# Kernel tuning notes

Hardware: AMD Instinct MI355X
Metric: run time of the kernel (lower is better)

Reference implementation:

```python
import jax, jax.numpy as jnp
import numpy as np

K = 4

def grid_sample_bilinear_zeros(img, grid):
    # img: [b,c,H,W]; grid: [b,h,w,2] normalized coords (x,y) in [-1,1]
    # PyTorch grid_sample, mode='bilinear', padding_mode='zeros', align_corners=False
    b, c, H, W = img.shape
    h, w = grid.shape[1], grid.shape[2]
    ix = (grid[..., 0] + 1.0) * (W * 0.5) - 0.5
    iy = (grid[..., 1] + 1.0) * (H * 0.5) - 0.5
    x0 = jnp.floor(ix); y0 = jnp.floor(iy)
    wx1 = ix - x0; wx0 = 1.0 - wx1
    wy1 = iy - y0; wy0 = 1.0 - wy1
    x0i = x0.astype(jnp.int32); y0i = y0.astype(jnp.int32)
    x1i = x0i + 1; y1i = y0i + 1
    imgf = img.reshape(b, c, H * W)
    N = h * w

    def gather(xi, yi, wgt):
        valid = (xi >= 0) & (xi < W) & (yi >= 0) & (yi < H)
        xc = jnp.clip(xi, 0, W - 1); yc = jnp.clip(yi, 0, H - 1)
        idx = (yc * W + xc).reshape(b, 1, N)
        g = jnp.take_along_axis(imgf, jnp.broadcast_to(idx, (b, c, N)), axis=2)
        wv = (wgt * valid.astype(img.dtype)).reshape(b, 1, N)
        return g * wv

    out = (gather(x0i, y0i, wx0 * wy0) + gather(x1i, y0i, wx1 * wy0) +
           gather(x0i, y1i, wx0 * wy1) + gather(x1i, y1i, wx1 * wy1))
    return out.reshape(b, c, h, w)


def setup_inputs() -> dict:
    key = jax.random.key(0)
    ks = jax.random.split(key, 8)
    b, c, h, w = 8, 256, 96, 96
    out_ch = 256
    x = jax.random.normal(ks[0], (b, c, h, w), dtype=jnp.float32)
    Wc = jax.random.normal(ks[1], (out_ch, c), dtype=jnp.float32) * 0.02
    bc = jax.random.normal(ks[2], (out_ch,), dtype=jnp.float32) * 0.02
    Woff = jax.random.normal(ks[3], (K, 2, c), dtype=jnp.float32) * 0.02
    boff = jax.random.normal(ks[4], (K, 2), dtype=jnp.float32) * 0.02
    Wwt = jax.random.normal(ks[5], (K, c), dtype=jnp.float32) * 0.02
    bwt = jax.random.normal(ks[6], (K,), dtype=jnp.float32) * 0.02
    return {"x": x, "Wc": Wc, "bc": bc, "Woff": Woff, "boff": boff, "Wwt": Wwt, "bwt": bwt}


def reference(x, Wc, bc, Woff, boff, Wwt, bwt):
    b, c, h, w = x.shape
    # 1x1 conv projection
    proj = jnp.einsum('bchw,oc->bohw', x, Wc) + bc[None, :, None, None]
    # k flow fields, each [b,2,h,w] -> [k,b,h,w,2]
    flows = jnp.einsum('bchw,koc->kbohw', x, Woff) + boff[:, None, :, None, None]
    flows = jnp.transpose(flows, (0, 1, 3, 4, 2))
    # softmax sampling weights [b,k,h,w]
    logits = jnp.einsum('bchw,kc->bkhw', x, Wwt) + bwt[None, :, None, None]
    weights = jax.nn.softmax(logits, axis=1)
    # base pixel grid (x,y)
    gy, gx = jnp.meshgrid(jnp.arange(h, dtype=x.dtype), jnp.arange(w, dtype=x.dtype), indexing='ij')
    base = jnp.stack((gx, gy), axis=-1)  # [h,w,2]
    vgrid = base[None, None] + flows  # [k,b,h,w,2]
    vx = 2.0 * vgrid[..., 0] / max(w - 1, 1) - 1.0
    vy = 2.0 * vgrid[..., 1] / max(h - 1, 1) - 1.0
    vgrid_scaled = jnp.stack((vx, vy), axis=-1)  # [k,b,h,w,2]
    feats = jax.vmap(lambda g: grid_sample_bilinear_zeros(proj, g))(vgrid_scaled)  # [k,b,o,h,w]
    out = jnp.einsum('kbohw,bkhw->bohw', feats, weights)
    return out
```

## Files before the change

kernel.cpp:

```cpp
#include <hip/hip_runtime.h>

#define HW   9216
#define IMG  96
#define NB   8
#define NK   4

typedef __bf16 bf16x8 __attribute__((ext_vector_type(8)));
typedef float  f32x4  __attribute__((ext_vector_type(4)));

__device__ __forceinline__ unsigned short f2bf(float f) {
    unsigned int u = __float_as_uint(f);
    u += 0x7FFFu + ((u >> 16) & 1u);
    return (unsigned short)(u >> 16);
}

extern "C" __global__ __launch_bounds__(256, 4)
void prep_kernel(const float* __restrict__ x,
                 const float* __restrict__ Wc,
                 const float* __restrict__ Woff,
                 const float* __restrict__ boff,
                 const float* __restrict__ Wwt,
                 const float* __restrict__ bwt,
                 unsigned short* __restrict__ xbt,
                 unsigned short* __restrict__ Wcb,
                 float2* __restrict__ coords,
                 float* __restrict__ wts)
{
    __shared__ __align__(16) unsigned short tile[64 * 264];

    const int t   = threadIdx.x;
    const int bxr = blockIdx.x;

    if (bxr >= NB * 144) {
        int u = ((bxr - NB * 144) * 256 + t) * 4;
        float4 v = *(const float4*)(Wc + u);
        union { unsigned short h[4]; int2 p; } pk;
        pk.h[0] = f2bf(v.x); pk.h[1] = f2bf(v.y);
        pk.h[2] = f2bf(v.z); pk.h[3] = f2bf(v.w);
        *(int2*)(Wcb + u) = pk.p;
        return;
    }

    const int b  = bxr / 144;
    const int p0 = (bxr % 144) * 64;
    const int px = t & 63;
    const int g  = __builtin_amdgcn_readfirstlane(t >> 6);

    float acc[12];
    #pragma unroll
    for (int j = 0; j < 12; ++j) acc[j] = 0.f;

    const float* xb = x + ((size_t)(b * 256 + g * 64)) * HW + p0 + px;
    unsigned int* trow = (unsigned int*)tile;

    for (int i0 = 0; i0 < 64; i0 += 8) {
        float v[8];
        #pragma unroll
        for (int q = 0; q < 8; ++q)
            v[q] = xb[(size_t)(i0 + q) * HW];
        #pragma unroll
        for (int q = 0; q < 8; ++q) {
            const int c = g * 64 + i0 + q;
            #pragma unroll
            for (int j = 0; j < 8; ++j) acc[j] += v[q] * Woff[j * 256 + c];
            #pragma unroll
            for (int j = 0; j < 4; ++j) acc[8 + j] += v[q] * Wwt[j * 256 + c];
        }
        #pragma unroll
        for (int q = 0; q < 8; q += 2) {
            unsigned int pk = (unsigned int)f2bf(v[q]) | ((unsigned int)f2bf(v[q + 1]) << 16);
            trow[px * 132 + ((g * 64 + i0 + q) >> 1)] = pk;
        }
    }

    __syncthreads();
    #pragma unroll
    for (int r = 0; r < 8; ++r) {
        int u = t + 256 * r;
        int sub = u & 31, p2 = u >> 5;
        int4 v = *(const int4*)(tile + p2 * 264 + sub * 8);
        *(int4*)(xbt + ((size_t)b * HW + p0 + p2) * 256 + sub * 8) = v;
    }
    __syncthreads();

    float* red = (float*)tile;
    #pragma unroll
    for (int j = 0; j < 12; ++j)
        red[(g * 64 + px) * 12 + j] = acc[j];
    __syncthreads();

    if (t < 64) {
        float s[12];
        #pragma unroll
        for (int j = 0; j < 12; ++j)
            s[j] = red[(0 * 64 + px) * 12 + j] + red[(1 * 64 + px) * 12 + j] +
                   red[(2 * 64 + px) * 12 + j] + red[(3 * 64 + px) * 12 + j];

        const int p = p0 + px;
        const float pyf = (float)(p / IMG);
        const float pxf = (float)(p % IMG);

        #pragma unroll
        for (int k = 0; k < NK; ++k) {
            float fx = s[k * 2 + 0] + boff[k * 2 + 0];
            float fy = s[k * 2 + 1] + boff[k * 2 + 1];
            float vx = 2.0f * (pxf + fx) / 95.0f - 1.0f;
            float vy = 2.0f * (pyf + fy) / 95.0f - 1.0f;
            float ix = (vx + 1.0f) * 48.0f - 0.5f;
            float iy = (vy + 1.0f) * 48.0f - 0.5f;
            coords[((size_t)k * NB + b) * HW + p] = make_float2(ix, iy);
        }
        float l0 = s[8] + bwt[0], l1 = s[9] + bwt[1];
        float l2 = s[10] + bwt[2], l3 = s[11] + bwt[3];
        float m = fmaxf(fmaxf(l0, l1), fmaxf(l2, l3));
        float e0 = __expf(l0 - m), e1 = __expf(l1 - m);
        float e2 = __expf(l2 - m), e3 = __expf(l3 - m);
        float inv = 1.0f / (e0 + e1 + e2 + e3);
        wts[((size_t)0 * NB + b) * HW + p] = e0 * inv;
        wts[((size_t)1 * NB + b) * HW + p] = e1 * inv;
        wts[((size_t)2 * NB + b) * HW + p] = e2 * inv;
        wts[((size_t)3 * NB + b) * HW + p] = e3 * inv;
    }
}

extern "C" __global__ __launch_bounds__(256)
void sample_kernel(const unsigned short* __restrict__ xbt,
                   const float2* __restrict__ coords,
                   float* __restrict__ wts,
                   unsigned short* __restrict__ xs)
{
    const int t  = threadIdx.x;
    const int b  = blockIdx.x / 1152;
    const int p0 = (blockIdx.x % 1152) * 8;
    const int pxl = t >> 5, ch = t & 31;
    const int p  = p0 + pxl;

    int   idx[16];
    float w[16];
    #pragma unroll
    for (int k = 0; k < NK; ++k) {
        float2 cc = coords[((size_t)k * NB + b) * HW + p];
        float wk  = wts[((size_t)k * NB + b) * HW + p];
        float x0f = floorf(cc.x), y0f = floorf(cc.y);
        float wx1 = cc.x - x0f, wx0 = 1.0f - wx1;
        float wy1 = cc.y - y0f, wy0 = 1.0f - wy1;
        int x0 = (int)x0f, y0 = (int)y0f;
        int x1 = x0 + 1,   y1 = y0 + 1;
        float vx0 = (x0 >= 0 && x0 < IMG) ? 1.f : 0.f;
        float vx1 = (x1 >= 0 && x1 < IMG) ? 1.f : 0.f;
        float vy0 = (y0 >= 0 && y0 < IMG) ? 1.f : 0.f;
        float vy1 = (y1 >= 0 && y1 < IMG) ? 1.f : 0.f;
        int cx0 = min(max(x0, 0), IMG - 1), cx1 = min(max(x1, 0), IMG - 1);
        int cy0 = min(max(y0, 0), IMG - 1), cy1 = min(max(y1, 0), IMG - 1);
        idx[k * 4 + 0] = cy0 * IMG + cx0;  w[k * 4 + 0] = wk * wx0 * wy0 * vx0 * vy0;
        idx[k * 4 + 1] = cy0 * IMG + cx1;  w[k * 4 + 1] = wk * wx1 * wy0 * vx1 * vy0;
        idx[k * 4 + 2] = cy1 * IMG + cx0;  w[k * 4 + 2] = wk * wx0 * wy1 * vx0 * vy1;
        idx[k * 4 + 3] = cy1 * IMG + cx1;  w[k * 4 + 3] = wk * wx1 * wy1 * vx1 * vy1;
    }

    const unsigned short* base = xbt + (size_t)b * HW * 256 + ch * 8;
    float acc[8];
    #pragma unroll
    for (int i = 0; i < 8; ++i) acc[i] = 0.f;

    #pragma unroll
    for (int j = 0; j < 16; ++j) {
        int4 v = *(const int4*)(base + (size_t)idx[j] * 256);
        const unsigned int* u = (const unsigned int*)&v;
        float wj = w[j];
        #pragma unroll
        for (int q = 0; q < 4; ++q) {
            float lo = __uint_as_float(u[q] << 16);
            float hi = __uint_as_float(u[q] & 0xFFFF0000u);
            acc[2 * q + 0] += wj * lo;
            acc[2 * q + 1] += wj * hi;
        }
    }

    union { unsigned short h[8]; int4 v; } pk;
    #pragma unroll
    for (int i = 0; i < 8; ++i) pk.h[i] = f2bf(acc[i]);
    *(int4*)(xs + ((size_t)b * HW + p) * 256 + ch * 8) = pk.v;

    if (ch == 0) {
        float wsum = 0.f;
        #pragma unroll
        for (int j = 0; j < 16; ++j) wsum += w[j];
        wts[(size_t)b * HW + p] = wsum;
    }
}

extern "C" __global__ __launch_bounds__(256)
void gemm_kernel(const unsigned short* __restrict__ Wcb,
                 const unsigned short* __restrict__ xs,
                 const float* __restrict__ bc,
                 const float* __restrict__ wts,
                 float* __restrict__ out)
{
    __shared__ __align__(16) unsigned short As[128 * 32];
    __shared__ __align__(16) unsigned short Bs[128 * 32];

    const int t  = threadIdx.x;
    const int bx = blockIdx.x;
    const int b  = bx / 144;
    const int r  = bx % 144;
    const int m0 = (r / 72) * 128;
    const int p0 = (r % 72) * 128;

    const int lane = t & 63, wave = t >> 6;
    const int wm = (wave >> 1) * 64, wn = (wave & 1) * 64;
    const int l15 = lane & 15, quad = lane >> 4;

    f32x4 acc[4][4];
    #pragma unroll
    for (int mt = 0; mt < 4; ++mt)
        #pragma unroll
        for (int nt = 0; nt < 4; ++nt)
            acc[mt][nt] = (f32x4){0.f, 0.f, 0.f, 0.f};

    const unsigned short* aBase = Wcb + (size_t)m0 * 256;
    const unsigned short* bBase = xs + ((size_t)b * HW + p0) * 256;

    for (int k0 = 0; k0 < 256; k0 += 32) {
        #pragma unroll
        for (int i = 0; i < 2; ++i) {
            int u = t + 256 * i;
            int row = u >> 2, sub = u & 3;
            __builtin_amdgcn_global_load_lds(
                (const __attribute__((address_space(1))) void*)(aBase + (size_t)row * 256 + k0 + sub * 8),
                (__attribute__((address_space(3))) void*)(As + u * 8), 16, 0, 0);
            __builtin_amdgcn_global_load_lds(
                (const __attribute__((address_space(1))) void*)(bBase + (size_t)row * 256 + k0 + sub * 8),
                (__attribute__((address_space(3))) void*)(Bs + u * 8), 16, 0, 0);
        }
        __syncthreads();
        bf16x8 af[4], bf[4];
        #pragma unroll
        for (int mt = 0; mt < 4; ++mt)
            af[mt] = *(const bf16x8*)(const void*)(As + (wm + mt * 16 + l15) * 32 + quad * 8);
        #pragma unroll
        for (int nt = 0; nt < 4; ++nt)
            bf[nt] = *(const bf16x8*)(const void*)(Bs + (wn + nt * 16 + l15) * 32 + quad * 8);
        #pragma unroll
        for (int mt = 0; mt < 4; ++mt)
            #pragma unroll
            for (int nt = 0; nt < 4; ++nt)
                acc[mt][nt] = __builtin_amdgcn_mfma_f32_16x16x32_bf16(af[mt], bf[nt], acc[mt][nt], 0, 0, 0);
        __syncthreads();
    }

    float wv[4];
    #pragma unroll
    for (int nt = 0; nt < 4; ++nt)
        wv[nt] = wts[(size_t)b * HW + p0 + wn + nt * 16 + l15];

    #pragma unroll
    for (int mt = 0; mt < 4; ++mt) {
        int ob = m0 + wm + mt * 16 + quad * 4;
        #pragma unroll
        for (int reg = 0; reg < 4; ++reg) {
            int o = ob + reg;
            float bias = bc[o];
            float* dst = out + ((size_t)b * 256 + o) * HW + p0 + wn + l15;
            #pragma unroll
            for (int nt = 0; nt < 4; ++nt)
                dst[nt * 16] = acc[mt][nt][reg] + bias * wv[nt];
        }
    }
}

extern "C" void kernel_launch(void* const* d_in, const int* in_sizes, int n_in,
                              void* d_out, int out_size, void* d_ws, size_t ws_size,
                              hipStream_t stream)
{
    const float* x    = (const float*)d_in[0];
    const float* Wc   = (const float*)d_in[1];
    const float* bc   = (const float*)d_in[2];
    const float* Woff = (const float*)d_in[3];
    const float* boff = (const float*)d_in[4];
    const float* Wwt  = (const float*)d_in[5];
    const float* bwt  = (const float*)d_in[6];
    float* out = (float*)d_out;

    char* ws = (char*)d_ws;
    unsigned short* xbt  = (unsigned short*)(ws);
    unsigned short* xs   = (unsigned short*)(ws + 37748736);
    float2* coords       = (float2*)(ws + 75497472);
    float*  wts          = (float*)(ws + 77856768);
    unsigned short* Wcb  = (unsigned short*)(ws + 79036416);

    prep_kernel<<<dim3(NB * 144 + 64), dim3(256), 0, stream>>>(
        x, Wc, Woff, boff, Wwt, bwt, xbt, Wcb, coords, wts);
    sample_kernel<<<dim3(NB * 1152), dim3(256), 0, stream>>>(xbt, coords, wts, xs);
    gemm_kernel<<<dim3(NB * 144), dim3(256), 0, stream>>>(Wcb, xs, bc, wts, out);
}
```

Measured before the change: 213.2 us.

## Stage x tiles via global_load_lds and write bf16 transpose directly

The prep kernel now loads x in two 32-channel phases per wave using direct global-to-LDS DMA loads with 16-byte vector accesses instead of strided per-thread scalar loads. Each lane reads its pixel column from LDS, accumulates the offset and weight projections, and writes its packed bf16 channel row straight to global memory. This removes the transposed LDS tile, one sync, and the cooperative copy-out loop. Launch bounds rise to 5 blocks per CU. Each lane's direct store covers only 16 bytes per row, and the hard vmcnt wait leaves the load and compute phases without overlap.

```diff
diff --git a/kernel.cpp b/kernel.cpp
--- a/kernel.cpp
+++ b/kernel.cpp
@@ -14,7 +14,7 @@
     return (unsigned short)(u >> 16);
 }
 
-extern "C" __global__ __launch_bounds__(256, 4)
+extern "C" __global__ __launch_bounds__(256, 5)
 void prep_kernel(const float* __restrict__ x,
                  const float* __restrict__ Wc,
                  const float* __restrict__ Woff,
@@ -26,7 +26,7 @@
                  float2* __restrict__ coords,
                  float* __restrict__ wts)
 {
-    __shared__ __align__(16) unsigned short tile[64 * 264];
+    __shared__ __align__(16) unsigned char lds_raw[32768];
 
     const int t   = threadIdx.x;
     const int bxr = blockIdx.x;
@@ -41,62 +41,70 @@
         return;
     }
 
-    const int b  = bxr / 144;
-    const int p0 = (bxr % 144) * 64;
-    const int px = t & 63;
-    const int g  = __builtin_amdgcn_readfirstlane(t >> 6);
+    const int b    = bxr / 144;
+    const int p0   = (bxr % 144) * 64;
+    const int lane = t & 63;
+    const int g    = __builtin_amdgcn_readfirstlane(t >> 6);
+
+    const float* XAf = (const float*)(lds_raw) + g * 2048;
 
     float acc[12];
     #pragma unroll
     for (int j = 0; j < 12; ++j) acc[j] = 0.f;
 
-    const float* xb = x + ((size_t)(b * 256 + g * 64)) * HW + p0 + px;
-    unsigned int* trow = (unsigned int*)tile;
-
-    for (int i0 = 0; i0 < 64; i0 += 8) {
-        float v[8];
-        #pragma unroll
-        for (int q = 0; q < 8; ++q)
-            v[q] = xb[(size_t)(i0 + q) * HW];
-        #pragma unroll
-        for (int q = 0; q < 8; ++q) {
-            const int c = g * 64 + i0 + q;
+    unsigned short* xrow = xbt + ((size_t)b * HW + p0 + lane) * 256 + g * 64;
+
+    #pragma unroll
+    for (int phase = 0; phase < 2; ++phase) {
+        const int cb = g * 64 + phase * 32;
+
+        #pragma unroll
+        for (int i2 = 0; i2 < 8; ++i2) {
+            const float* src = x + ((size_t)(b * 256 + cb + i2 * 4 + (lane >> 4))) * HW
+                                 + p0 + (lane & 15) * 4;
+            __builtin_amdgcn_global_load_lds(
+                (const __attribute__((address_space(1))) void*)src,
+                (__attribute__((address_space(3))) void*)(lds_raw + g * 8192 + i2 * 1024 + lane * 16),
+                16, 0, 0);
+        }
+        asm volatile("s_waitcnt vmcnt(0)" ::: "memory");
+
+        #pragma unroll
+        for (int s8 = 0; s8 < 4; ++s8) {
+            union { unsigned int u[4]; int4 i4; } pk;
             #pragma unroll
-            for (int j = 0; j < 8; ++j) acc[j] += v[q] * Woff[j * 256 + c];
-            #pragma unroll
-            for (int j = 0; j < 4; ++j) acc[8 + j] += v[q] * Wwt[j * 256 + c];
-        }
-        #pragma unroll
-        for (int q = 0; q < 8; q += 2) {
-            unsigned int pk = (unsigned int)f2bf(v[q]) | ((unsigned int)f2bf(v[q + 1]) << 16);
-            trow[px * 132 + ((g * 64 + i0 + q) >> 1)] = pk;
+            for (int pr = 0; pr < 4; ++pr) {
+                const int r = s8 * 8 + pr * 2;
+                float v0 = XAf[(r + 0) * 64 + lane];
+                float v1 = XAf[(r + 1) * 64 + lane];
+                const int c0 = cb + r, c1 = cb + r + 1;
+                #pragma unroll
+                for (int j = 0; j < 8; ++j)
+                    acc[j] += v0 * Woff[j * 256 + c0] + v1 * Woff[j * 256 + c1];
+                #pragma unroll
+                for (int j = 0; j < 4; ++j)
+                    acc[8 + j] += v0 * Wwt[j * 256 + c0] + v1 * Wwt[j * 256 + c1];
+                pk.u[pr] = (unsigned int)f2bf(v0) | ((unsigned int)f2bf(v1) << 16);
+            }
+            *(int4*)(xrow + phase * 32 + s8 * 8) = pk.i4;
         }
     }
 
     __syncthreads();
-    #pragma unroll
-    for (int r = 0; r < 8; ++r) {
-        int u = t + 256 * r;
-        int sub = u & 31, p2 = u >> 5;
-        int4 v = *(const int4*)(tile + p2 * 264 + sub * 8);
-        *(int4*)(xbt + ((size_t)b * HW + p0 + p2) * 256 + sub * 8) = v;
-    }
-    __syncthreads();
-
-    float* red = (float*)tile;
+    float* red = (float*)lds_raw;
     #pragma unroll
     for (int j = 0; j < 12; ++j)
-        red[(g * 64 + px) * 12 + j] = acc[j];
+        red[(g * 64 + lane) * 12 + j] = acc[j];
     __syncthreads();
 
     if (t < 64) {
         float s[12];
         #pragma unroll
         for (int j = 0; j < 12; ++j)
-            s[j] = red[(0 * 64 + px) * 12 + j] + red[(1 * 64 + px) * 12 + j] +
-                   red[(2 * 64 + px) * 12 + j] + red[(3 * 64 + px) * 12 + j];
-
-        const int p = p0 + px;
+            s[j] = red[(0 * 64 + lane) * 12 + j] + red[(1 * 64 + lane) * 12 + j] +
+                   red[(2 * 64 + lane) * 12 + j] + red[(3 * 64 + lane) * 12 + j];
+
+        const int p = p0 + lane;
         const float pyf = (float)(p / IMG);
         const float pxf = (float)(p % IMG);
 
```

Measured after the change: 232.5 us. 1.09x slower.

## Fuse bilinear sampling into GEMM kernel, staging sampled tile in LDS

Applied to the files above, without the earlier changes.

Merges the sampling kernel into the GEMM: each block computes sampling indices and weights for its 128 pixels, gathers and blends all 256 input channels into a swizzled LDS B tile, then runs the MFMA loop reading only A from global memory. This removes the bf16 intermediate write and re-read and one kernel launch. The cost is that the two output-channel halves each redo the full gather for the same pixels, and the large LDS footprint limits occupancy. XOR swizzles are added to A and B LDS layouts to reduce bank conflicts.

```diff
diff --git a/kernel.cpp b/kernel.cpp
--- a/kernel.cpp
+++ b/kernel.cpp
@@ -123,82 +123,20 @@
     }
 }
 
-extern "C" __global__ __launch_bounds__(256)
-void sample_kernel(const unsigned short* __restrict__ xbt,
-                   const float2* __restrict__ coords,
-                   float* __restrict__ wts,
-                   unsigned short* __restrict__ xs)
+extern "C" __global__ __launch_bounds__(256, 2)
+void fused_kernel(const unsigned short* __restrict__ Wcb,
+                  const unsigned short* __restrict__ xbt,
+                  const float2* __restrict__ coords,
+                  const float* __restrict__ wts,
+                  const float* __restrict__ bc,
+                  float* __restrict__ out)
 {
-    const int t  = threadIdx.x;
-    const int b  = blockIdx.x / 1152;
-    const int p0 = (blockIdx.x % 1152) * 8;
-    const int pxl = t >> 5, ch = t & 31;
-    const int p  = p0 + pxl;
-
-    int   idx[16];
-    float w[16];
-    #pragma unroll
-    for (int k = 0; k < NK; ++k) {
-        float2 cc = coords[((size_t)k * NB + b) * HW + p];
-        float wk  = wts[((size_t)k * NB + b) * HW + p];
-        float x0f = floorf(cc.x), y0f = floorf(cc.y);
-        float wx1 = cc.x - x0f, wx0 = 1.0f - wx1;
-        float wy1 = cc.y - y0f, wy0 = 1.0f - wy1;
-        int x0 = (int)x0f, y0 = (int)y0f;
-        int x1 = x0 + 1,   y1 = y0 + 1;
-        float vx0 = (x0 >= 0 && x0 < IMG) ? 1.f : 0.f;
-        float vx1 = (x1 >= 0 && x1 < IMG) ? 1.f : 0.f;
-        float vy0 = (y0 >= 0 && y0 < IMG) ? 1.f : 0.f;
-        float vy1 = (y1 >= 0 && y1 < IMG) ? 1.f : 0.f;
-        int cx0 = min(max(x0, 0), IMG - 1), cx1 = min(max(x1, 0), IMG - 1);
-        int cy0 = min(max(y0, 0), IMG - 1), cy1 = min(max(y1, 0), IMG - 1);
-        idx[k * 4 + 0] = cy0 * IMG + cx0;  w[k * 4 + 0] = wk * wx0 * wy0 * vx0 * vy0;
-        idx[k * 4 + 1] = cy0 * IMG + cx1;  w[k * 4 + 1] = wk * wx1 * wy0 * vx1 * vy0;
-        idx[k * 4 + 2] = cy1 * IMG + cx0;  w[k * 4 + 2] = wk * wx0 * wy1 * vx0 * vy1;
-        idx[k * 4 + 3] = cy1 * IMG + cx1;  w[k * 4 + 3] = wk * wx1 * wy1 * vx1 * vy1;
-    }
-
-    const unsigned short* base = xbt + (size_t)b * HW * 256 + ch * 8;
-    float acc[8];
-    #pragma unroll
-    for (int i = 0; i < 8; ++i) acc[i] = 0.f;
-
-    #pragma unroll
-    for (int j = 0; j < 16; ++j) {
-        int4 v = *(const int4*)(base + (size_t)idx[j] * 256);
-        const unsigned int* u = (const unsigned int*)&v;
-        float wj = w[j];
-        #pragma unroll
-        for (int q = 0; q < 4; ++q) {
-            float lo = __uint_as_float(u[q] << 16);
-            float hi = __uint_as_float(u[q] & 0xFFFF0000u);
-            acc[2 * q + 0] += wj * lo;
-            acc[2 * q + 1] += wj * hi;
-        }
-    }
-
-    union { unsigned short h[8]; int4 v; } pk;
-    #pragma unroll
-    for (int i = 0; i < 8; ++i) pk.h[i] = f2bf(acc[i]);
-    *(int4*)(xs + ((size_t)b * HW + p) * 256 + ch * 8) = pk.v;
-
-    if (ch == 0) {
-        float wsum = 0.f;
-        #pragma unroll
-        for (int j = 0; j < 16; ++j) wsum += w[j];
-        wts[(size_t)b * HW + p] = wsum;
-    }
-}
-
-extern "C" __global__ __launch_bounds__(256)
-void gemm_kernel(const unsigned short* __restrict__ Wcb,
-                 const unsigned short* __restrict__ xs,
-                 const float* __restrict__ bc,
-                 const float* __restrict__ wts,
-                 float* __restrict__ out)
-{
-    __shared__ __align__(16) unsigned short As[128 * 32];
-    __shared__ __align__(16) unsigned short Bs[128 * 32];
+    __shared__ __align__(16) unsigned char lds[78336];
+    unsigned short* BsU  = (unsigned short*)lds;
+    unsigned short* AsU  = (unsigned short*)(lds + 65536);
+    float*          cw   = (float*)(lds + 65536);
+    unsigned int*   ci   = (unsigned int*)(lds + 65536 + 8192);
+    float*          wsumL= (float*)(lds + 77824);
 
     const int t  = threadIdx.x;
     const int bx = blockIdx.x;
@@ -207,6 +145,93 @@
     const int m0 = (r / 72) * 128;
     const int p0 = (r % 72) * 128;
 
+    if (t < 128) {
+        const int px = t;
+        const int p  = p0 + px;
+        float wsum_acc = 0.f;
+        #pragma unroll
+        for (int k = 0; k < NK; ++k) {
+            float2 cc = coords[((size_t)k * NB + b) * HW + p];
+            float wk  = wts[((size_t)k * NB + b) * HW + p];
+            float x0f = floorf(cc.x), y0f = floorf(cc.y);
+            float wx1 = cc.x - x0f, wx0 = 1.0f - wx1;
+            float wy1 = cc.y - y0f, wy0 = 1.0f - wy1;
+            int x0 = (int)x0f, y0 = (int)y0f;
+            int x1 = x0 + 1,   y1 = y0 + 1;
+            float vx0 = (x0 >= 0 && x0 < IMG) ? 1.f : 0.f;
+            float vx1 = (x1 >= 0 && x1 < IMG) ? 1.f : 0.f;
+            float vy0 = (y0 >= 0 && y0 < IMG) ? 1.f : 0.f;
+            float vy1 = (y1 >= 0 && y1 < IMG) ? 1.f : 0.f;
+            int cx0 = min(max(x0, 0), IMG - 1), cx1 = min(max(x1, 0), IMG - 1);
+            int cy0 = min(max(y0, 0), IMG - 1), cy1 = min(max(y1, 0), IMG - 1);
+            int i0 = cy0 * IMG + cx0, i1 = cy0 * IMG + cx1;
+            int i2 = cy1 * IMG + cx0, i3 = cy1 * IMG + cx1;
+            float w0 = wk * wx0 * wy0 * vx0 * vy0;
+            float w1 = wk * wx1 * wy0 * vx1 * vy0;
+            float w2 = wk * wx0 * wy1 * vx0 * vy1;
+            float w3 = wk * wx1 * wy1 * vx1 * vy1;
+            float4 wv4 = make_float4(w0, w1, w2, w3);
+            *(float4*)(cw + px * 16 + k * 4) = wv4;
+            uint2 ip;
+            ip.x = (unsigned int)i0 | ((unsigned int)i1 << 16);
+            ip.y = (unsigned int)i2 | ((unsigned int)i3 << 16);
+            *(uint2*)(ci + px * 8 + k * 2) = ip;
+            wsum_acc += w0 + w1 + w2 + w3;
+        }
+        wsumL[px] = wsum_acc;
+    }
+    __syncthreads();
+
+    {
+        const int pxl = t >> 5, ch = t & 31;
+        const unsigned short* gbase = xbt + (size_t)b * HW * 256 + ch * 8;
+        #pragma unroll 2
+        for (int rep = 0; rep < 16; ++rep) {
+            const int px = rep * 8 + pxl;
+            float wl[16];
+            #pragma unroll
+            for (int q = 0; q < 4; ++q) {
+                float4 wv = *(const float4*)(cw + px * 16 + q * 4);
+                wl[q * 4 + 0] = wv.x; wl[q * 4 + 1] = wv.y;
+                wl[q * 4 + 2] = wv.z; wl[q * 4 + 3] = wv.w;
+            }
+            unsigned int ip[8];
+            #pragma unroll
+            for (int q = 0; q < 2; ++q) {
+                uint4 iv = *(const uint4*)(ci + px * 8 + q * 4);
+                ip[q * 4 + 0] = iv.x; ip[q * 4 + 1] = iv.y;
+                ip[q * 4 + 2] = iv.z; ip[q * 4 + 3] = iv.w;
+            }
+            int4 v[16];
+            #pragma unroll
+            for (int j = 0; j < 16; ++j) {
+                unsigned int idx = (ip[j >> 1] >> ((j & 1) * 16)) & 0xFFFFu;
+                v[j] = *(const int4*)(gbase + (size_t)idx * 256);
+            }
+            float acc[8];
+            #pragma unroll
+            for (int i = 0; i < 8; ++i) acc[i] = 0.f;
+            #pragma unroll
+            for (int j = 0; j < 16; ++j) {
+                const unsigned int* u = (const unsigned int*)&v[j];
+                float wj = wl[j];
+                #pragma unroll
+                for (int q = 0; q < 4; ++q) {
+                    float lo = __uint_as_float(u[q] << 16);
+                    float hi = __uint_as_float(u[q] & 0xFFFF0000u);
+                    acc[2 * q + 0] += wj * lo;
+                    acc[2 * q + 1] += wj * hi;
+                }
+            }
+            union { unsigned short h[8]; int4 v4; } pk;
+            #pragma unroll
+            for (int i = 0; i < 8; ++i) pk.h[i] = f2bf(acc[i]);
+            const int pos = ch ^ (px & 7);
+            *(int4*)(BsU + px * 256 + pos * 8) = pk.v4;
+        }
+    }
+    __syncthreads();
+
     const int lane = t & 63, wave = t >> 6;
     const int wm = (wave >> 1) * 64, wn = (wave & 1) * 64;
     const int l15 = lane & 15, quad = lane >> 4;
@@ -219,28 +244,31 @@
             acc[mt][nt] = (f32x4){0.f, 0.f, 0.f, 0.f};
 
     const unsigned short* aBase = Wcb + (size_t)m0 * 256;
-    const unsigned short* bBase = xs + ((size_t)b * HW + p0) * 256;
 
     for (int k0 = 0; k0 < 256; k0 += 32) {
         #pragma unroll
         for (int i = 0; i < 2; ++i) {
             int u = t + 256 * i;
             int row = u >> 2, sub = u & 3;
+            int sub_g = sub ^ ((row >> 1) & 3);
             __builtin_amdgcn_global_load_lds(
-                (const __attribute__((address_space(1))) void*)(aBase + (size_t)row * 256 + k0 + sub * 8),
-                (__attribute__((address_space(3))) void*)(As + u * 8), 16, 0, 0);
-            __builtin_amdgcn_global_load_lds(
-                (const __attribute__((address_space(1))) void*)(bBase + (size_t)row * 256 + k0 + sub * 8),
-                (__attribute__((address_space(3))) void*)(Bs + u * 8), 16, 0, 0);
+                (const __attribute__((address_space(1))) void*)(aBase + (size_t)row * 256 + k0 + sub_g * 8),
+                (__attribute__((address_space(3))) void*)(AsU + u * 8), 16, 0, 0);
         }
         __syncthreads();
         bf16x8 af[4], bf[4];
         #pragma unroll
-        for (int mt = 0; mt < 4; ++mt)
-            af[mt] = *(const bf16x8*)(const void*)(As + (wm + mt * 16 + l15) * 32 + quad * 8);
-        #pragma unroll
-        for (int nt = 0; nt < 4; ++nt)
-            bf[nt] = *(const bf16x8*)(const void*)(Bs + (wn + nt * 16 + l15) * 32 + quad * 8);
+        for (int mt = 0; mt < 4; ++mt) {
+            int row = wm + mt * 16 + l15;
+            int cch = quad ^ ((row >> 1) & 3);
+            af[mt] = *(const bf16x8*)(const void*)(AsU + row * 32 + cch * 8);
+        }
+        #pragma unroll
+        for (int nt = 0; nt < 4; ++nt) {
+            int row = wn + nt * 16 + l15;
+            int pos = ((k0 >> 3) + quad) ^ (row & 7);
+            bf[nt] = *(const bf16x8*)(const void*)(BsU + row * 256 + pos * 8);
+        }
         #pragma unroll
         for (int mt = 0; mt < 4; ++mt)
             #pragma unroll
@@ -252,7 +280,7 @@
     float wv[4];
     #pragma unroll
     for (int nt = 0; nt < 4; ++nt)
-        wv[nt] = wts[(size_t)b * HW + p0 + wn + nt * 16 + l15];
+        wv[nt] = wsumL[wn + nt * 16 + l15];
 
     #pragma unroll
     for (int mt = 0; mt < 4; ++mt) {
@@ -284,13 +312,12 @@
 
     char* ws = (char*)d_ws;
     unsigned short* xbt  = (unsigned short*)(ws);
-    unsigned short* xs   = (unsigned short*)(ws + 37748736);
     float2* coords       = (float2*)(ws + 75497472);
     float*  wts          = (float*)(ws + 77856768);
     unsigned short* Wcb  = (unsigned short*)(ws + 79036416);
 
     prep_kernel<<<dim3(NB * 144 + 64), dim3(256), 0, stream>>>(
         x, Wc, Woff, boff, Wwt, bwt, xbt, Wcb, coords, wts);
-    sample_kernel<<<dim3(NB * 1152), dim3(256), 0, stream>>>(xbt, coords, wts, xs);
-    gemm_kernel<<<dim3(NB * 144), dim3(256), 0, stream>>>(Wcb, xs, bc, wts, out);
+    fused_kernel<<<dim3(NB * 144), dim3(256), 0, stream>>>(
+        Wcb, xbt, coords, wts, bc, out);
 }
```

After: 211.5 us. About the same (-0.8%).
